# Performance work log

Measured on AMD Instinct MI355X. Metric: run time of the kernel, lower is better.

The kernel has to match this reference:

```python
import jax, jax.numpy as jnp
import numpy as np

C_IN = 192
HEADS = 6
QKV_DIM = C_IN // HEADS  # 32
WH = WW = 4              # window_size
PAD_H = WH // 2          # 2
PAD_W = WW // 2          # 2


def setup_inputs() -> dict:
    key = jax.random.key(0)
    ks = jax.random.split(key, 6)
    s = 0.02
    return {
        "x": jax.random.normal(ks[0], (8, C_IN, 128, 128), jnp.float32),
        "w_qkv1": jax.random.normal(ks[1], (3 * C_IN, C_IN), jnp.float32) * s,
        "b_qkv1": jnp.zeros((3 * C_IN,), jnp.float32),
        "w_qkv2": jax.random.normal(ks[2], (3 * C_IN, C_IN), jnp.float32) * s,
        "b_qkv2": jnp.zeros((3 * C_IN,), jnp.float32),
        "w_head": jax.random.normal(ks[3], (C_IN, 2 * C_IN), jnp.float32) * s,  # 1x1 conv as matmul
        "b_head": jnp.zeros((C_IN,), jnp.float32),
    }


def _window_partition(x):
    # bchw_to_bnc: [B,C,H,W] -> [B*nh*nw, WH*WW, C]
    B, C, H, W = x.shape
    nh, nw = H // WH, W // WW
    x = x.reshape(B, C, nh, WH, nw, WW)
    x = x.transpose(0, 2, 4, 3, 5, 1)  # B,nh,nw,WH,WW,C
    return x.reshape(B * nh * nw, WH * WW, C)


def _window_merge(x, out_shape):
    # bnc_to_bchw: inverse of _window_partition
    B, C, H, W = out_shape
    nh, nw = H // WH, W // WW
    x = x.reshape(B, nh, nw, WH, WW, C)
    x = x.transpose(0, 5, 1, 3, 2, 4)  # B,C,nh,WH,nw,WW
    return x.reshape(B, C, H, W)


def _mha(xw, w, b):
    # xw: [Bn, N=16, C]; fused QKV projection then per-window SDPA
    Bn, N, C = xw.shape
    qkv = xw @ w.T + b
    q, k, v = jnp.split(qkv, 3, axis=-1)
    to_heads = lambda t: t.reshape(Bn, N, HEADS, QKV_DIM).transpose(0, 2, 1, 3)
    q, k, v = to_heads(q), to_heads(k), to_heads(v)
    scale = 1.0 / np.sqrt(QKV_DIM).astype(np.float32)
    attn = jax.nn.softmax(jnp.einsum('bhnd,bhmd->bhnm', q, k) * scale, axis=-1)
    o = jnp.einsum('bhnm,bhmd->bhnd', attn, v)
    return o.transpose(0, 2, 1, 3).reshape(Bn, N, C)


def reference(x, w_qkv1, b_qkv1, w_qkv2, b_qkv2, w_head, b_head):
    # branch 2: zero-pad by window//2 on each side (shifted windows)
    x2 = jnp.pad(x, ((0, 0), (0, 0), (PAD_H, PAD_H), (PAD_W, PAD_W)))
    s1, s2 = x.shape, x2.shape
    o1 = _window_merge(_mha(_window_partition(x), w_qkv1, b_qkv1), s1)
    o2 = _window_merge(_mha(_window_partition(x2), w_qkv2, b_qkv2), s2)
    o2 = o2[:, :, PAD_H:-PAD_H, PAD_W:-PAD_W]  # negative pad = crop
    o = jnp.concatenate([o1, o2], axis=1)      # [B, 2C, H, W]
    # 1x1 conv head projection
    return jnp.einsum('bchw,oc->bohw', o, w_head) + b_head[None, :, None, None]
```

## Files before the change

kernel.cpp:

```cpp
#include <hip/hip_runtime.h>


typedef unsigned short u16;
using bf16x8 = __attribute__((ext_vector_type(8))) short;
using f32x4  = __attribute__((ext_vector_type(4))) float;
using u16x8  = __attribute__((ext_vector_type(8))) unsigned short;
using u16x4  = __attribute__((ext_vector_type(4))) unsigned short;

#define CIN   192
#define NW2   33
#define QSCALE 0.17677669529663687f

__device__ __forceinline__ u16 f2bf(float f) {
    unsigned int x; __builtin_memcpy(&x, &f, 4);
    return (u16)((x + 0x7FFFu + ((x >> 16) & 1u)) >> 16);
}
__device__ __forceinline__ int xcol(int c, int tok) {
    int blk = (c >> 3) ^ ((tok ^ (tok >> 4)) & 7);
    return blk * 8 + (c & 7);
}

__global__ void prep_w(const float* __restrict__ w1, const float* __restrict__ w2,
                       const float* __restrict__ wh,
                       u16* __restrict__ w1b, u16* __restrict__ w2b,
                       u16* __restrict__ whb) {
    int i = blockIdx.x * 256 + threadIdx.x;
    if (i < 221184) {
        int j = (i < 110592) ? i : i - 110592;
        int co = j / 192;
        float v = ((i < 110592) ? w1 : w2)[j];
        if (co < 192) v *= QSCALE;
        ((i < 110592) ? w1b : w2b)[j] = f2bf(v);
    } else if (i < 294912) {
        int j = i - 221184;
        whb[j] = f2bf(wh[j]);
    }
}

__global__ __launch_bounds__(256, 2) void prep_x(const float* __restrict__ x,
                                                 u16* __restrict__ xp) {
    __shared__ __align__(16) u16 lt[128 * 200];
    int bi = blockIdx.x;
    int b = bi / 132, hp = bi % 132;
    u16* orow = xp + ((size_t)(b * 132 + hp)) * 132 * 192;
    const int tid = threadIdx.x;

    if (hp >= 2 && hp < 130) {
        const int h = hp - 2;
        const float* xr = x + (size_t)b * 192 * 128 * 128 + (size_t)h * 128;
#pragma unroll
        for (int it = 0; it < 24; ++it) {
            int i = it * 256 + tid;
            int c = i >> 5, w0 = (i & 31) * 4;
            float4 v = *reinterpret_cast<const float4*>(&xr[(size_t)c * 16384 + w0]);
            lt[(w0 + 0) * 200 + xcol(c, w0 + 0)] = f2bf(v.x);
            lt[(w0 + 1) * 200 + xcol(c, w0 + 1)] = f2bf(v.y);
            lt[(w0 + 2) * 200 + xcol(c, w0 + 2)] = f2bf(v.z);
            lt[(w0 + 3) * 200 + xcol(c, w0 + 3)] = f2bf(v.w);
        }
        __syncthreads();
#pragma unroll
        for (int it = 0; it < 13; ++it) {
            int i = it * 256 + tid;
            if (i < 3168) {
                int wp = i / 24, kc = i - wp * 24;
                u16x8 val = {};
                if (wp >= 2 && wp < 130) {
                    int w = wp - 2;
                    int blk = kc ^ ((w ^ (w >> 4)) & 7);
                    val = *reinterpret_cast<const u16x8*>(&lt[w * 200 + blk * 8]);
                }
                *reinterpret_cast<u16x8*>(&orow[(size_t)wp * 192 + kc * 8]) = val;
            }
        }
    } else {
#pragma unroll
        for (int it = 0; it < 13; ++it) {
            int i = it * 256 + tid;
            if (i < 3168) {
                u16x8 z = {};
                *reinterpret_cast<u16x8*>(&orow[(size_t)i * 8]) = z;
            }
        }
    }
}

__device__ __forceinline__ void attn_tail(f32x4 (&acc)[9][4],
                                          const float* __restrict__ bias,
                                          u16* qk, u16* vt, u16* pl,
                                          int wave, int lane, int lo16, int quad,
                                          bool br0, int b, int wy, int g,
                                          u16* __restrict__ ocat) {
#pragma unroll
    for (int mt = 0; mt < 9; ++mt) {
        int co0 = wave * 144 + mt * 16 + quad * 4;
        float4 bv = *reinterpret_cast<const float4*>(&bias[co0]);
        if (co0 < 192) { bv.x *= QSCALE; bv.y *= QSCALE; bv.z *= QSCALE; bv.w *= QSCALE; }
#pragma unroll
        for (int nt = 0; nt < 4; ++nt) {
            int tok = nt * 16 + lo16;
            float v0 = acc[mt][nt][0] + bv.x, v1 = acc[mt][nt][1] + bv.y;
            float v2 = acc[mt][nt][2] + bv.z, v3 = acc[mt][nt][3] + bv.w;
            if (co0 < 384) {
                u16x4 pk = {f2bf(v0), f2bf(v1), f2bf(v2), f2bf(v3)};
                *reinterpret_cast<u16x4*>(&qk[tok * 392 + co0]) = pk;
            } else {
                int dh = co0 - 384;
                int head = dh >> 5, d0 = dh & 31;
                int win = tok >> 4, m = tok & 15;
                u16* vrow = &vt[((win * 6 + head) * 32 + d0) * 16 + m];
                vrow[0]  = f2bf(v0);
                vrow[16] = f2bf(v1);
                vrow[32] = f2bf(v2);
                vrow[48] = f2bf(v3);
            }
        }
    }
    __syncthreads();

    const int win = wave;
    const u16* qbase = qk + (size_t)(win * 16) * 392;
    const bf16x8 z8 = {};
    const f32x4 zc = {0.f, 0.f, 0.f, 0.f};
    bool dov; size_t dst = 0;
    if (br0) {
        int wg = wy * 32 + g * 4 + win;
        dst = (((size_t)(b * 1024 + wg)) * 16 + lo16) * 384;
        dov = true;
    } else {
        int wx = g * 4 + win;
        int h = wy * 4 + (lo16 >> 2) - 2;
        int w = wx * 4 + (lo16 & 3) - 2;
        dov = (wx < NW2) && (unsigned)h < 128u && (unsigned)w < 128u;
        if (dov) {
            int wg = (h >> 2) * 32 + (w >> 2);
            int nn = (h & 3) * 4 + (w & 3);
            dst = (((size_t)(b * 1024 + wg)) * 16 + nn) * 384 + 192;
        }
    }
#pragma unroll
    for (int head = 0; head < 6; ++head) {
        bf16x8 kfr = *reinterpret_cast<const bf16x8*>(
            &qbase[lo16 * 392 + 192 + head * 32 + quad * 8]);
        bf16x8 qfr = *reinterpret_cast<const bf16x8*>(
            &qbase[lo16 * 392 + head * 32 + quad * 8]);
        f32x4 st = __builtin_amdgcn_mfma_f32_16x16x32_bf16(kfr, qfr, zc, 0, 0, 0);
        float mx = fmaxf(fmaxf(st[0], st[1]), fmaxf(st[2], st[3]));
        mx = fmaxf(mx, __shfl_xor(mx, 16));
        mx = fmaxf(mx, __shfl_xor(mx, 32));
        float p0 = __expf(st[0] - mx), p1 = __expf(st[1] - mx);
        float p2 = __expf(st[2] - mx), p3 = __expf(st[3] - mx);
        float sum = p0 + p1 + p2 + p3;
        sum += __shfl_xor(sum, 16);
        sum += __shfl_xor(sum, 32);
        float inv = 1.0f / sum;
        u16x4 pk = {f2bf(p0), f2bf(p1), f2bf(p2), f2bf(p3)};
        *reinterpret_cast<u16x4*>(&pl[(wave * 16 + lo16) * 24 + quad * 4]) = pk;
        bf16x8 pf = (quad < 2)
            ? *reinterpret_cast<const bf16x8*>(&pl[(wave * 16 + lo16) * 24 + quad * 8]) : z8;
        const u16* vbase = &vt[(win * 6 + head) * 32 * 16];
#pragma unroll
        for (int half = 0; half < 2; ++half) {
            bf16x8 av = (quad < 2)
                ? *reinterpret_cast<const bf16x8*>(&vbase[(half * 16 + lo16) * 16 + quad * 8]) : z8;
            f32x4 o = __builtin_amdgcn_mfma_f32_16x16x32_bf16(av, pf, zc, 0, 0, 0);
            if (dov) {
                u16x4 ok = {f2bf(o[0] * inv), f2bf(o[1] * inv),
                            f2bf(o[2] * inv), f2bf(o[3] * inv)};
                *reinterpret_cast<u16x4*>(&ocat[dst + head * 32 + half * 16 + quad * 4]) = ok;
            }
        }
    }
}

__global__ __launch_bounds__(256, 2) void qkv_attn_g(const u16* __restrict__ xp,
                                                     const u16* __restrict__ w1b,
                                                     const float* __restrict__ b1,
                                                     const u16* __restrict__ w2b,
                                                     const float* __restrict__ b2,
                                                     u16* __restrict__ ocat) {
    __shared__ __align__(16) char smem[77824];
    u16* qk = (u16*)smem;
    u16* vt = (u16*)(smem + 50176);
    u16* pl = (u16*)(smem + 74752);

    const int tid  = threadIdx.x;
    const int wave = tid >> 6, lane = tid & 63;
    const int lo16 = lane & 15, quad = lane >> 4;

    const int swz = (blockIdx.x & 7) * 553 + (blockIdx.x >> 3);
    const bool br0 = (swz < 2048);

    int b, wy, g;
    const u16* wb; const float* bias;
    if (br0) { b = swz >> 8; int rem = swz & 255; wy = rem >> 3; g = rem & 7;
               wb = w1b; bias = b1; }
    else     { int bi = swz - 2048; b = bi / 297; int rem = bi % 297;
               wy = rem / 9; g = rem % 9; wb = w2b; bias = b2; }

    const int d  = br0 ? 2 : 0;
    const int ty = lo16 >> 2, tx = lo16 & 3;
    const u16* bp[4];
#pragma unroll
    for (int nt = 0; nt < 4; ++nt) {
        int wx = g * 4 + nt;
        if (!br0 && wx > 32) wx = 32;
        int hp = d + wy * 4 + ty;
        int wp = d + wx * 4 + tx;
        bp[nt] = xp + (((size_t)b * 132 + hp) * 132 + wp) * 192 + quad * 8;
    }

    f32x4 acc[9][4];
#pragma unroll
    for (int mt = 0; mt < 9; ++mt)
#pragma unroll
        for (int nt = 0; nt < 4; ++nt) acc[mt][nt] = f32x4{0.f, 0.f, 0.f, 0.f};

    const u16* wrow = wb + (size_t)(wave * 144 + lo16) * 192 + quad * 8;
#pragma unroll
    for (int s = 0; s < 6; ++s) {
        bf16x8 bfr[4];
#pragma unroll
        for (int nt = 0; nt < 4; ++nt)
            bfr[nt] = *reinterpret_cast<const bf16x8*>(bp[nt] + s * 32);
#pragma unroll
        for (int mt = 0; mt < 9; ++mt) {
            bf16x8 afr = *reinterpret_cast<const bf16x8*>(&wrow[mt * 3072 + s * 32]);
#pragma unroll
            for (int nt = 0; nt < 4; ++nt)
                acc[mt][nt] = __builtin_amdgcn_mfma_f32_16x16x32_bf16(afr, bfr[nt], acc[mt][nt], 0, 0, 0);
        }
    }
    attn_tail(acc, bias, qk, vt, pl, wave, lane, lo16, quad, br0, b, wy, g, ocat);
}

__global__ __launch_bounds__(256, 2) void qkv_attn_fb(const float* __restrict__ x,
                                                      const u16* __restrict__ w1b,
                                                      const float* __restrict__ b1,
                                                      const u16* __restrict__ w2b,
                                                      const float* __restrict__ b2,
                                                      u16* __restrict__ ocat) {
    __shared__ __align__(16) char smem[77824];
    u16* xl = (u16*)smem;
    u16* qk = (u16*)smem;
    u16* vt = (u16*)(smem + 50176);
    u16* pl = (u16*)(smem + 74752);

    const int tid  = threadIdx.x;
    const int wave = tid >> 6, lane = tid & 63;
    const int lo16 = lane & 15, quad = lane >> 4;

    const int swz = (blockIdx.x & 7) * 553 + (blockIdx.x >> 3);
    const bool br0 = (swz < 2048);

    int b, wy, g;
    const u16* wb; const float* bias;
    if (br0) { b = swz >> 8; int rem = swz & 255; wy = rem >> 3; g = rem & 7;
               wb = w1b; bias = b1; }
    else     { int bi = swz - 2048; b = bi / 297; int rem = bi % 297;
               wy = rem / 9; g = rem % 9; wb = w2b; bias = b2; }
    const int hbase = wy * 4, wbase = g * 16;

    if (br0) {
#pragma unroll
        for (int it = 0; it < 12; ++it) {
            int i = it * 256 + tid;
            int c = i >> 4, y = (i >> 2) & 3, xc = i & 3;
            const float4 v = *reinterpret_cast<const float4*>(
                &x[(((size_t)b * CIN + c) * 128 + hbase + y) * 128 + wbase + xc * 4]);
            int t0 = xc * 16 + y * 4;
            xl[(t0 + 0) * 200 + xcol(c, t0 + 0)] = f2bf(v.x);
            xl[(t0 + 1) * 200 + xcol(c, t0 + 1)] = f2bf(v.y);
            xl[(t0 + 2) * 200 + xcol(c, t0 + 2)] = f2bf(v.z);
            xl[(t0 + 3) * 200 + xcol(c, t0 + 3)] = f2bf(v.w);
        }
    } else {
#pragma unroll
        for (int it = 0; it < 12; ++it) {
            int i = it * 256 + tid;
            int c = i >> 4, y = (i >> 2) & 3, xc = i & 3;
            float e0, e1, e2, e3;
            int h = hbase + y - 2;
            int w0 = wbase + xc * 4 - 2;
            bool hok = (unsigned)h < 128u;
            const float* row = &x[(((size_t)b * CIN + c) * 128 + h) * 128];
            if (hok && w0 >= 0 && w0 + 3 < 128) {
                float2 p0 = *reinterpret_cast<const float2*>(&row[w0]);
                float2 p1 = *reinterpret_cast<const float2*>(&row[w0 + 2]);
                e0 = p0.x; e1 = p0.y; e2 = p1.x; e3 = p1.y;
            } else {
                e0 = (hok && w0 >= 0 && w0 < 128)         ? row[w0]     : 0.f;
                e1 = (hok && w0+1 >= 0 && w0+1 < 128)     ? row[w0 + 1] : 0.f;
                e2 = (hok && w0+2 >= 0 && w0+2 < 128)     ? row[w0 + 2] : 0.f;
                e3 = (hok && w0+3 >= 0 && w0+3 < 128)     ? row[w0 + 3] : 0.f;
            }
            int t0 = xc * 16 + y * 4;
            xl[(t0 + 0) * 200 + xcol(c, t0 + 0)] = f2bf(e0);
            xl[(t0 + 1) * 200 + xcol(c, t0 + 1)] = f2bf(e1);
            xl[(t0 + 2) * 200 + xcol(c, t0 + 2)] = f2bf(e2);
            xl[(t0 + 3) * 200 + xcol(c, t0 + 3)] = f2bf(e3);
        }
    }
    __syncthreads();

    f32x4 acc[9][4];
#pragma unroll
    for (int mt = 0; mt < 9; ++mt)
#pragma unroll
        for (int nt = 0; nt < 4; ++nt) acc[mt][nt] = f32x4{0.f, 0.f, 0.f, 0.f};

    const u16* wrow = wb + (size_t)(wave * 144 + lo16) * 192 + quad * 8;
#pragma unroll
    for (int s = 0; s < 6; ++s) {
        bf16x8 bfr[4];
#pragma unroll
        for (int nt = 0; nt < 4; ++nt) {
            int tok = nt * 16 + lo16;
            int kb = s * 4 + quad;
            bfr[nt] = *reinterpret_cast<const bf16x8*>(
                &xl[tok * 200 + (((kb ^ ((tok ^ (tok >> 4)) & 7)) << 3))]);
        }
#pragma unroll
        for (int mt = 0; mt < 9; ++mt) {
            bf16x8 afr = *reinterpret_cast<const bf16x8*>(&wrow[mt * 3072 + s * 32]);
#pragma unroll
            for (int nt = 0; nt < 4; ++nt)
                acc[mt][nt] = __builtin_amdgcn_mfma_f32_16x16x32_bf16(afr, bfr[nt], acc[mt][nt], 0, 0, 0);
        }
    }
    __syncthreads();
    attn_tail(acc, bias, qk, vt, pl, wave, lane, lo16, quad, br0, b, wy, g, ocat);
}

__global__ __launch_bounds__(256, 6) void head_gemm(const u16* __restrict__ ocat,
                                                    const u16* __restrict__ whb,
                                                    const float* __restrict__ bh,
                                                    float* __restrict__ out) {
    __shared__ __align__(16) u16 bt[32 * 392];
    const int tid = threadIdx.x;
    const int wave = tid >> 6, lane = tid & 63;
    const int lo16 = lane & 15, quad = lane >> 4;

    int bi = (blockIdx.x & 7) * 512 + (blockIdx.x >> 3);
    int b = bi >> 9; int rem = bi & 511;
    int wy = rem >> 4, g = rem & 15;
    const int wg0 = wy * 32 + g * 2;
    const size_t gbase = ((size_t)(b * 1024 + wg0) * 16) * 384;

#pragma unroll
    for (int it = 0; it < 6; ++it) {
        int i = it * 256 + tid;
        u16x8 v = *reinterpret_cast<const u16x8*>(&ocat[gbase + (size_t)i * 8]);
        int row = i / 48, kc = i - row * 48;
        *reinterpret_cast<u16x8*>(&bt[row * 392 + kc * 8]) = v;
    }
    __syncthreads();

    const int co_base = wave * 48;
    f32x4 acc[3][2];
#pragma unroll
    for (int mt = 0; mt < 3; ++mt)
#pragma unroll
        for (int nt = 0; nt < 2; ++nt) acc[mt][nt] = f32x4{0.f, 0.f, 0.f, 0.f};

#pragma unroll
    for (int s = 0; s < 12; ++s) {
        int k0 = s * 32;
        bf16x8 a[3], bb[2];
#pragma unroll
        for (int nt = 0; nt < 2; ++nt)
            bb[nt] = *reinterpret_cast<const bf16x8*>(&bt[(nt * 16 + lo16) * 392 + k0 + quad * 8]);
#pragma unroll
        for (int mt = 0; mt < 3; ++mt)
            a[mt] = *reinterpret_cast<const bf16x8*>(
                &whb[(size_t)(co_base + mt * 16 + lo16) * 384 + k0 + quad * 8]);
#pragma unroll
        for (int mt = 0; mt < 3; ++mt)
#pragma unroll
            for (int nt = 0; nt < 2; ++nt)
                acc[mt][nt] = __builtin_amdgcn_mfma_f32_16x16x32_bf16(a[mt], bb[nt], acc[mt][nt], 0, 0, 0);
    }

    int h = wy * 4 + (lo16 >> 2);
#pragma unroll
    for (int mt = 0; mt < 3; ++mt) {
        int co0 = co_base + mt * 16 + quad * 4;
        const float4 bv = *reinterpret_cast<const float4*>(&bh[co0]);
#pragma unroll
        for (int r = 0; r < 4; ++r) {
            float bias = (r == 0) ? bv.x : (r == 1) ? bv.y : (r == 2) ? bv.z : bv.w;
#pragma unroll
            for (int nt = 0; nt < 2; ++nt) {
                int w = (g * 2 + nt) * 4 + (lo16 & 3);
                out[(((size_t)b * CIN + co0 + r) * 128 + h) * 128 + w] = acc[mt][nt][r] + bias;
            }
        }
    }
}

extern "C" void kernel_launch(void* const* d_in, const int* in_sizes, int n_in,
                              void* d_out, int out_size, void* d_ws, size_t ws_size,
                              hipStream_t stream) {
    const float* x  = (const float*)d_in[0];
    const float* w1 = (const float*)d_in[1];
    const float* b1 = (const float*)d_in[2];
    const float* w2 = (const float*)d_in[3];
    const float* b2 = (const float*)d_in[4];
    const float* wh = (const float*)d_in[5];
    const float* bh = (const float*)d_in[6];
    float* out = (float*)d_out;

    char* ws = (char*)d_ws;
    u16* ocat = (u16*)ws;
    u16* w1b  = (u16*)(ws + 100663296);
    u16* w2b  = (u16*)(ws + 100884480);
    u16* whb  = (u16*)(ws + 101105664);
    u16* xp   = (u16*)(ws + 101253120);

    const size_t need_full = 101253120u + 53526528u;

    prep_w<<<1152, 256, 0, stream>>>(w1, w2, wh, w1b, w2b, whb);
    if (ws_size >= need_full) {
        prep_x<<<1056, 256, 0, stream>>>(x, xp);
        qkv_attn_g<<<4424, 256, 0, stream>>>(xp, w1b, b1, w2b, b2, ocat);
    } else {
        qkv_attn_fb<<<4424, 256, 0, stream>>>(x, w1b, b1, w2b, b2, ocat);
    }
    head_gemm<<<4096, 256, 0, stream>>>(ocat, whb, bh, out);
}
```

Before: 495.0 us.

## Split QKV-attention work across 8 waves and drop LDS staging in head GEMM

The fused QKV projection and window-attention kernel now uses 512-thread blocks. Each wave computes half the token tile (144x32 outputs), and in the attention phase each wave handles three heads of one window. This halves per-wave accumulator registers to raise latency hiding and parallelism, at the cost of more threads per block and slightly more shared memory. The head projection GEMM now reads ocat fragments directly from global memory instead of staging them through LDS with a barrier, and its launch bound occupancy hint is lowered. The old attn_tail helper is inlined into the fallback kernel.

```diff
diff --git a/kernel.cpp b/kernel.cpp
--- a/kernel.cpp
+++ b/kernel.cpp
@@ -85,20 +85,72 @@
     }
 }
 
-__device__ __forceinline__ void attn_tail(f32x4 (&acc)[9][4],
-                                          const float* __restrict__ bias,
-                                          u16* qk, u16* vt, u16* pl,
-                                          int wave, int lane, int lo16, int quad,
-                                          bool br0, int b, int wy, int g,
-                                          u16* __restrict__ ocat) {
+__global__ __launch_bounds__(512, 2) void qkv_attn_g2(const u16* __restrict__ xp,
+                                                      const u16* __restrict__ w1b,
+                                                      const float* __restrict__ b1,
+                                                      const u16* __restrict__ w2b,
+                                                      const float* __restrict__ b2,
+                                                      u16* __restrict__ ocat) {
+    __shared__ __align__(16) char smem[80896];
+    u16* qk = (u16*)smem;
+    u16* vt = (u16*)(smem + 50176);
+    u16* pl = (u16*)(smem + 74752);
+
+    const int tid  = threadIdx.x;
+    const int wave = tid >> 6, lane = tid & 63;
+    const int lo16 = lane & 15, quad = lane >> 4;
+    const int wm = wave >> 1, wn = wave & 1;
+
+    const int swz = (blockIdx.x & 7) * 553 + (blockIdx.x >> 3);
+    const bool br0 = (swz < 2048);
+
+    int b, wy, g;
+    const u16* wb; const float* bias;
+    if (br0) { b = swz >> 8; int rem = swz & 255; wy = rem >> 3; g = rem & 7;
+               wb = w1b; bias = b1; }
+    else     { int bi = swz - 2048; b = bi / 297; int rem = bi % 297;
+               wy = rem / 9; g = rem % 9; wb = w2b; bias = b2; }
+
+    const int d  = br0 ? 2 : 0;
+    const int ty = lo16 >> 2, tx = lo16 & 3;
+    const u16* bp[2];
+#pragma unroll
+    for (int nt = 0; nt < 2; ++nt) {
+        int wx = g * 4 + wn * 2 + nt;
+        if (!br0 && wx > 32) wx = 32;
+        int hp = d + wy * 4 + ty;
+        int wp = d + wx * 4 + tx;
+        bp[nt] = xp + (((size_t)b * 132 + hp) * 132 + wp) * 192 + quad * 8;
+    }
+
+    f32x4 acc[9][2];
+#pragma unroll
+    for (int mt = 0; mt < 9; ++mt)
+#pragma unroll
+        for (int nt = 0; nt < 2; ++nt) acc[mt][nt] = f32x4{0.f, 0.f, 0.f, 0.f};
+
+    const u16* wrow = wb + (size_t)(wm * 144 + lo16) * 192 + quad * 8;
+#pragma unroll
+    for (int s = 0; s < 6; ++s) {
+        bf16x8 bfr[2];
+        bfr[0] = *reinterpret_cast<const bf16x8*>(bp[0] + s * 32);
+        bfr[1] = *reinterpret_cast<const bf16x8*>(bp[1] + s * 32);
+#pragma unroll
+        for (int mt = 0; mt < 9; ++mt) {
+            bf16x8 afr = *reinterpret_cast<const bf16x8*>(&wrow[mt * 3072 + s * 32]);
+            acc[mt][0] = __builtin_amdgcn_mfma_f32_16x16x32_bf16(afr, bfr[0], acc[mt][0], 0, 0, 0);
+            acc[mt][1] = __builtin_amdgcn_mfma_f32_16x16x32_bf16(afr, bfr[1], acc[mt][1], 0, 0, 0);
+        }
+    }
+
 #pragma unroll
     for (int mt = 0; mt < 9; ++mt) {
-        int co0 = wave * 144 + mt * 16 + quad * 4;
+        int co0 = wm * 144 + mt * 16 + quad * 4;
         float4 bv = *reinterpret_cast<const float4*>(&bias[co0]);
         if (co0 < 192) { bv.x *= QSCALE; bv.y *= QSCALE; bv.z *= QSCALE; bv.w *= QSCALE; }
 #pragma unroll
-        for (int nt = 0; nt < 4; ++nt) {
-            int tok = nt * 16 + lo16;
+        for (int nt = 0; nt < 2; ++nt) {
+            int tok = wn * 32 + nt * 16 + lo16;
             float v0 = acc[mt][nt][0] + bv.x, v1 = acc[mt][nt][1] + bv.y;
             float v2 = acc[mt][nt][2] + bv.z, v3 = acc[mt][nt][3] + bv.w;
             if (co0 < 384) {
@@ -118,120 +170,63 @@
     }
     __syncthreads();
 
-    const int win = wave;
-    const u16* qbase = qk + (size_t)(win * 16) * 392;
-    const bf16x8 z8 = {};
-    const f32x4 zc = {0.f, 0.f, 0.f, 0.f};
-    bool dov; size_t dst = 0;
-    if (br0) {
-        int wg = wy * 32 + g * 4 + win;
-        dst = (((size_t)(b * 1024 + wg)) * 16 + lo16) * 384;
-        dov = true;
-    } else {
-        int wx = g * 4 + win;
-        int h = wy * 4 + (lo16 >> 2) - 2;
-        int w = wx * 4 + (lo16 & 3) - 2;
-        dov = (wx < NW2) && (unsigned)h < 128u && (unsigned)w < 128u;
-        if (dov) {
-            int wg = (h >> 2) * 32 + (w >> 2);
-            int nn = (h & 3) * 4 + (w & 3);
-            dst = (((size_t)(b * 1024 + wg)) * 16 + nn) * 384 + 192;
-        }
-    }
-#pragma unroll
-    for (int head = 0; head < 6; ++head) {
-        bf16x8 kfr = *reinterpret_cast<const bf16x8*>(
-            &qbase[lo16 * 392 + 192 + head * 32 + quad * 8]);
-        bf16x8 qfr = *reinterpret_cast<const bf16x8*>(
-            &qbase[lo16 * 392 + head * 32 + quad * 8]);
-        f32x4 st = __builtin_amdgcn_mfma_f32_16x16x32_bf16(kfr, qfr, zc, 0, 0, 0);
-        float mx = fmaxf(fmaxf(st[0], st[1]), fmaxf(st[2], st[3]));
-        mx = fmaxf(mx, __shfl_xor(mx, 16));
-        mx = fmaxf(mx, __shfl_xor(mx, 32));
-        float p0 = __expf(st[0] - mx), p1 = __expf(st[1] - mx);
-        float p2 = __expf(st[2] - mx), p3 = __expf(st[3] - mx);
-        float sum = p0 + p1 + p2 + p3;
-        sum += __shfl_xor(sum, 16);
-        sum += __shfl_xor(sum, 32);
-        float inv = 1.0f / sum;
-        u16x4 pk = {f2bf(p0), f2bf(p1), f2bf(p2), f2bf(p3)};
-        *reinterpret_cast<u16x4*>(&pl[(wave * 16 + lo16) * 24 + quad * 4]) = pk;
-        bf16x8 pf = (quad < 2)
-            ? *reinterpret_cast<const bf16x8*>(&pl[(wave * 16 + lo16) * 24 + quad * 8]) : z8;
-        const u16* vbase = &vt[(win * 6 + head) * 32 * 16];
-#pragma unroll
-        for (int half = 0; half < 2; ++half) {
-            bf16x8 av = (quad < 2)
-                ? *reinterpret_cast<const bf16x8*>(&vbase[(half * 16 + lo16) * 16 + quad * 8]) : z8;
-            f32x4 o = __builtin_amdgcn_mfma_f32_16x16x32_bf16(av, pf, zc, 0, 0, 0);
+    {
+        const int win = wave >> 1;
+        const int h0  = (wave & 1) * 3;
+        const u16* qbase = qk + (size_t)(win * 16) * 392;
+        const bf16x8 z8 = {};
+        const f32x4 zc = {0.f, 0.f, 0.f, 0.f};
+        bool dov; size_t dst = 0;
+        if (br0) {
+            int wg = wy * 32 + g * 4 + win;
+            dst = (((size_t)(b * 1024 + wg)) * 16 + lo16) * 384;
+            dov = true;
+        } else {
+            int wx = g * 4 + win;
+            int h = wy * 4 + (lo16 >> 2) - 2;
+            int w = wx * 4 + (lo16 & 3) - 2;
+            dov = (wx < NW2) && (unsigned)h < 128u && (unsigned)w < 128u;
             if (dov) {
-                u16x4 ok = {f2bf(o[0] * inv), f2bf(o[1] * inv),
-                            f2bf(o[2] * inv), f2bf(o[3] * inv)};
-                *reinterpret_cast<u16x4*>(&ocat[dst + head * 32 + half * 16 + quad * 4]) = ok;
-            }
-        }
-    }
-}
-
-__global__ __launch_bounds__(256, 2) void qkv_attn_g(const u16* __restrict__ xp,
-                                                     const u16* __restrict__ w1b,
-                                                     const float* __restrict__ b1,
-                                                     const u16* __restrict__ w2b,
-                                                     const float* __restrict__ b2,
-                                                     u16* __restrict__ ocat) {
-    __shared__ __align__(16) char smem[77824];
-    u16* qk = (u16*)smem;
-    u16* vt = (u16*)(smem + 50176);
-    u16* pl = (u16*)(smem + 74752);
-
-    const int tid  = threadIdx.x;
-    const int wave = tid >> 6, lane = tid & 63;
-    const int lo16 = lane & 15, quad = lane >> 4;
-
-    const int swz = (blockIdx.x & 7) * 553 + (blockIdx.x >> 3);
-    const bool br0 = (swz < 2048);
-
-    int b, wy, g;
-    const u16* wb; const float* bias;
-    if (br0) { b = swz >> 8; int rem = swz & 255; wy = rem >> 3; g = rem & 7;
-               wb = w1b; bias = b1; }
-    else     { int bi = swz - 2048; b = bi / 297; int rem = bi % 297;
-               wy = rem / 9; g = rem % 9; wb = w2b; bias = b2; }
-
-    const int d  = br0 ? 2 : 0;
-    const int ty = lo16 >> 2, tx = lo16 & 3;
-    const u16* bp[4];
-#pragma unroll
-    for (int nt = 0; nt < 4; ++nt) {
-        int wx = g * 4 + nt;
-        if (!br0 && wx > 32) wx = 32;
-        int hp = d + wy * 4 + ty;
-        int wp = d + wx * 4 + tx;
-        bp[nt] = xp + (((size_t)b * 132 + hp) * 132 + wp) * 192 + quad * 8;
-    }
-
-    f32x4 acc[9][4];
-#pragma unroll
-    for (int mt = 0; mt < 9; ++mt)
-#pragma unroll
-        for (int nt = 0; nt < 4; ++nt) acc[mt][nt] = f32x4{0.f, 0.f, 0.f, 0.f};
-
-    const u16* wrow = wb + (size_t)(wave * 144 + lo16) * 192 + quad * 8;
-#pragma unroll
-    for (int s = 0; s < 6; ++s) {
-        bf16x8 bfr[4];
-#pragma unroll
-        for (int nt = 0; nt < 4; ++nt)
-            bfr[nt] = *reinterpret_cast<const bf16x8*>(bp[nt] + s * 32);
-#pragma unroll
-        for (int mt = 0; mt < 9; ++mt) {
-            bf16x8 afr = *reinterpret_cast<const bf16x8*>(&wrow[mt * 3072 + s * 32]);
-#pragma unroll
-            for (int nt = 0; nt < 4; ++nt)
-                acc[mt][nt] = __builtin_amdgcn_mfma_f32_16x16x32_bf16(afr, bfr[nt], acc[mt][nt], 0, 0, 0);
-        }
-    }
-    attn_tail(acc, bias, qk, vt, pl, wave, lane, lo16, quad, br0, b, wy, g, ocat);
+                int wg = (h >> 2) * 32 + (w >> 2);
+                int nn = (h & 3) * 4 + (w & 3);
+                dst = (((size_t)(b * 1024 + wg)) * 16 + nn) * 384 + 192;
+            }
+        }
+#pragma unroll
+        for (int hh = 0; hh < 3; ++hh) {
+            const int head = h0 + hh;
+            bf16x8 kfr = *reinterpret_cast<const bf16x8*>(
+                &qbase[lo16 * 392 + 192 + head * 32 + quad * 8]);
+            bf16x8 qfr = *reinterpret_cast<const bf16x8*>(
+                &qbase[lo16 * 392 + head * 32 + quad * 8]);
+            f32x4 st = __builtin_amdgcn_mfma_f32_16x16x32_bf16(kfr, qfr, zc, 0, 0, 0);
+            float mx = fmaxf(fmaxf(st[0], st[1]), fmaxf(st[2], st[3]));
+            mx = fmaxf(mx, __shfl_xor(mx, 16));
+            mx = fmaxf(mx, __shfl_xor(mx, 32));
+            float p0 = __expf(st[0] - mx), p1 = __expf(st[1] - mx);
+            float p2 = __expf(st[2] - mx), p3 = __expf(st[3] - mx);
+            float sum = p0 + p1 + p2 + p3;
+            sum += __shfl_xor(sum, 16);
+            sum += __shfl_xor(sum, 32);
+            float inv = 1.0f / sum;
+            u16x4 pk = {f2bf(p0), f2bf(p1), f2bf(p2), f2bf(p3)};
+            *reinterpret_cast<u16x4*>(&pl[(wave * 16 + lo16) * 24 + quad * 4]) = pk;
+            bf16x8 pf = (quad < 2)
+                ? *reinterpret_cast<const bf16x8*>(&pl[(wave * 16 + lo16) * 24 + quad * 8]) : z8;
+            const u16* vbase = &vt[(win * 6 + head) * 32 * 16];
+#pragma unroll
+            for (int half = 0; half < 2; ++half) {
+                bf16x8 av = (quad < 2)
+                    ? *reinterpret_cast<const bf16x8*>(&vbase[(half * 16 + lo16) * 16 + quad * 8]) : z8;
+                f32x4 o = __builtin_amdgcn_mfma_f32_16x16x32_bf16(av, pf, zc, 0, 0, 0);
+                if (dov) {
+                    u16x4 ok = {f2bf(o[0] * inv), f2bf(o[1] * inv),
+                                f2bf(o[2] * inv), f2bf(o[3] * inv)};
+                    *reinterpret_cast<u16x4*>(&ocat[dst + head * 32 + half * 16 + quad * 4]) = ok;
+                }
+            }
+        }
+    }
 }
 
 __global__ __launch_bounds__(256, 2) void qkv_attn_fb(const float* __restrict__ x,
@@ -329,14 +324,95 @@
         }
     }
     __syncthreads();
-    attn_tail(acc, bias, qk, vt, pl, wave, lane, lo16, quad, br0, b, wy, g, ocat);
-}
-
-__global__ __launch_bounds__(256, 6) void head_gemm(const u16* __restrict__ ocat,
+
+#pragma unroll
+    for (int mt = 0; mt < 9; ++mt) {
+        int co0 = wave * 144 + mt * 16 + quad * 4;
+        float4 bv = *reinterpret_cast<const float4*>(&bias[co0]);
+        if (co0 < 192) { bv.x *= QSCALE; bv.y *= QSCALE; bv.z *= QSCALE; bv.w *= QSCALE; }
+#pragma unroll
+        for (int nt = 0; nt < 4; ++nt) {
+            int tok = nt * 16 + lo16;
+            float v0 = acc[mt][nt][0] + bv.x, v1 = acc[mt][nt][1] + bv.y;
+            float v2 = acc[mt][nt][2] + bv.z, v3 = acc[mt][nt][3] + bv.w;
+            if (co0 < 384) {
+                u16x4 pk = {f2bf(v0), f2bf(v1), f2bf(v2), f2bf(v3)};
+                *reinterpret_cast<u16x4*>(&qk[tok * 392 + co0]) = pk;
+            } else {
+                int dh = co0 - 384;
+                int head = dh >> 5, d0 = dh & 31;
+                int win = tok >> 4, m = tok & 15;
+                u16* vrow = &vt[((win * 6 + head) * 32 + d0) * 16 + m];
+                vrow[0]  = f2bf(v0);
+                vrow[16] = f2bf(v1);
+                vrow[32] = f2bf(v2);
+                vrow[48] = f2bf(v3);
+            }
+        }
+    }
+    __syncthreads();
+
+    {
+        const int win = wave;
+        const u16* qbase = qk + (size_t)(win * 16) * 392;
+        const bf16x8 z8 = {};
+        const f32x4 zc = {0.f, 0.f, 0.f, 0.f};
+        bool dov; size_t dst = 0;
+        if (br0) {
+            int wg = wy * 32 + g * 4 + win;
+            dst = (((size_t)(b * 1024 + wg)) * 16 + lo16) * 384;
+            dov = true;
+        } else {
+            int wx = g * 4 + win;
+            int h = wy * 4 + (lo16 >> 2) - 2;
+            int w = wx * 4 + (lo16 & 3) - 2;
+            dov = (wx < NW2) && (unsigned)h < 128u && (unsigned)w < 128u;
+            if (dov) {
+                int wg = (h >> 2) * 32 + (w >> 2);
+                int nn = (h & 3) * 4 + (w & 3);
+                dst = (((size_t)(b * 1024 + wg)) * 16 + nn) * 384 + 192;
+            }
+        }
+#pragma unroll
+        for (int head = 0; head < 6; ++head) {
+            bf16x8 kfr = *reinterpret_cast<const bf16x8*>(
+                &qbase[lo16 * 392 + 192 + head * 32 + quad * 8]);
+            bf16x8 qfr = *reinterpret_cast<const bf16x8*>(
+                &qbase[lo16 * 392 + head * 32 + quad * 8]);
+            f32x4 st = __builtin_amdgcn_mfma_f32_16x16x32_bf16(kfr, qfr, zc, 0, 0, 0);
+            float mx = fmaxf(fmaxf(st[0], st[1]), fmaxf(st[2], st[3]));
+            mx = fmaxf(mx, __shfl_xor(mx, 16));
+            mx = fmaxf(mx, __shfl_xor(mx, 32));
+            float p0 = __expf(st[0] - mx), p1 = __expf(st[1] - mx);
+            float p2 = __expf(st[2] - mx), p3 = __expf(st[3] - mx);
+            float sum = p0 + p1 + p2 + p3;
+            sum += __shfl_xor(sum, 16);
+            sum += __shfl_xor(sum, 32);
+            float inv = 1.0f / sum;
+            u16x4 pk = {f2bf(p0), f2bf(p1), f2bf(p2), f2bf(p3)};
+            *reinterpret_cast<u16x4*>(&pl[(wave * 16 + lo16) * 24 + quad * 4]) = pk;
+            bf16x8 pf = (quad < 2)
+                ? *reinterpret_cast<const bf16x8*>(&pl[(wave * 16 + lo16) * 24 + quad * 8]) : z8;
+            const u16* vbase = &vt[(win * 6 + head) * 32 * 16];
+#pragma unroll
+            for (int half = 0; half < 2; ++half) {
+                bf16x8 av = (quad < 2)
+                    ? *reinterpret_cast<const bf16x8*>(&vbase[(half * 16 + lo16) * 16 + quad * 8]) : z8;
+                f32x4 o = __builtin_amdgcn_mfma_f32_16x16x32_bf16(av, pf, zc, 0, 0, 0);
+                if (dov) {
+                    u16x4 ok = {f2bf(o[0] * inv), f2bf(o[1] * inv),
+                                f2bf(o[2] * inv), f2bf(o[3] * inv)};
+                    *reinterpret_cast<u16x4*>(&ocat[dst + head * 32 + half * 16 + quad * 4]) = ok;
+                }
+            }
+        }
+    }
+}
+
+__global__ __launch_bounds__(256, 4) void head_gemm(const u16* __restrict__ ocat,
                                                     const u16* __restrict__ whb,
                                                     const float* __restrict__ bh,
                                                     float* __restrict__ out) {
-    __shared__ __align__(16) u16 bt[32 * 392];
     const int tid = threadIdx.x;
     const int wave = tid >> 6, lane = tid & 63;
     const int lo16 = lane & 15, quad = lane >> 4;
@@ -347,16 +423,10 @@
     const int wg0 = wy * 32 + g * 2;
     const size_t gbase = ((size_t)(b * 1024 + wg0) * 16) * 384;
 
-#pragma unroll
-    for (int it = 0; it < 6; ++it) {
-        int i = it * 256 + tid;
-        u16x8 v = *reinterpret_cast<const u16x8*>(&ocat[gbase + (size_t)i * 8]);
-        int row = i / 48, kc = i - row * 48;
-        *reinterpret_cast<u16x8*>(&bt[row * 392 + kc * 8]) = v;
-    }
-    __syncthreads();
-
-    const int co_base = wave * 48;
+    const u16* brow0 = ocat + gbase + (size_t)lo16 * 384 + quad * 8;
+    const u16* brow1 = brow0 + 16 * 384;
+    const u16* arow  = whb + (size_t)(wave * 48 + lo16) * 384 + quad * 8;
+
     f32x4 acc[3][2];
 #pragma unroll
     for (int mt = 0; mt < 3; ++mt)
@@ -366,22 +436,21 @@
 #pragma unroll
     for (int s = 0; s < 12; ++s) {
         int k0 = s * 32;
-        bf16x8 a[3], bb[2];
-#pragma unroll
-        for (int nt = 0; nt < 2; ++nt)
-            bb[nt] = *reinterpret_cast<const bf16x8*>(&bt[(nt * 16 + lo16) * 392 + k0 + quad * 8]);
-#pragma unroll
-        for (int mt = 0; mt < 3; ++mt)
-            a[mt] = *reinterpret_cast<const bf16x8*>(
-                &whb[(size_t)(co_base + mt * 16 + lo16) * 384 + k0 + quad * 8]);
-#pragma unroll
-        for (int mt = 0; mt < 3; ++mt)
-#pragma unroll
-            for (int nt = 0; nt < 2; ++nt)
-                acc[mt][nt] = __builtin_amdgcn_mfma_f32_16x16x32_bf16(a[mt], bb[nt], acc[mt][nt], 0, 0, 0);
+        bf16x8 a0 = *reinterpret_cast<const bf16x8*>(arow + k0);
+        bf16x8 a1 = *reinterpret_cast<const bf16x8*>(arow + 16 * 384 + k0);
+        bf16x8 a2 = *reinterpret_cast<const bf16x8*>(arow + 32 * 384 + k0);
+        bf16x8 b0 = *reinterpret_cast<const bf16x8*>(brow0 + k0);
+        bf16x8 b1 = *reinterpret_cast<const bf16x8*>(brow1 + k0);
+        acc[0][0] = __builtin_amdgcn_mfma_f32_16x16x32_bf16(a0, b0, acc[0][0], 0, 0, 0);
+        acc[0][1] = __builtin_amdgcn_mfma_f32_16x16x32_bf16(a0, b1, acc[0][1], 0, 0, 0);
+        acc[1][0] = __builtin_amdgcn_mfma_f32_16x16x32_bf16(a1, b0, acc[1][0], 0, 0, 0);
+        acc[1][1] = __builtin_amdgcn_mfma_f32_16x16x32_bf16(a1, b1, acc[1][1], 0, 0, 0);
+        acc[2][0] = __builtin_amdgcn_mfma_f32_16x16x32_bf16(a2, b0, acc[2][0], 0, 0, 0);
+        acc[2][1] = __builtin_amdgcn_mfma_f32_16x16x32_bf16(a2, b1, acc[2][1], 0, 0, 0);
     }
 
     int h = wy * 4 + (lo16 >> 2);
+    const int co_base = wave * 48;
 #pragma unroll
     for (int mt = 0; mt < 3; ++mt) {
         int co0 = co_base + mt * 16 + quad * 4;
@@ -422,7 +491,7 @@
     prep_w<<<1152, 256, 0, stream>>>(w1, w2, wh, w1b, w2b, whb);
     if (ws_size >= need_full) {
         prep_x<<<1056, 256, 0, stream>>>(x, xp);
-        qkv_attn_g<<<4424, 256, 0, stream>>>(xp, w1b, b1, w2b, b2, ocat);
+        qkv_attn_g2<<<4424, 512, 0, stream>>>(xp, w1b, b1, w2b, b2, ocat);
     } else {
         qkv_attn_fb<<<4424, 256, 0, stream>>>(x, w1b, b1, w2b, b2, ocat);
     }
```

Result: slower. 651.9 us (+31.7%).
